# Kernel optimization log

Hardware: AMD Instinct MI355X
Metric: run time of the kernel (lower is better)

## Reference

```python
import jax, jax.numpy as jnp
import numpy as np

N_NODES = 100000
N_EDGES = 1600000
NFEAT = 256
NHID = 128


def setup_inputs() -> dict:
    key = jax.random.key(0)
    ks = jax.random.split(key, 8)
    x = jax.random.normal(ks[0], (N_NODES, NFEAT), dtype=jnp.float32)
    edge_row = jax.random.randint(ks[1], (N_EDGES,), 0, N_NODES, dtype=jnp.int32)
    edge_col = jax.random.randint(ks[2], (N_EDGES,), 0, N_NODES, dtype=jnp.int32)
    edge_val = jax.random.uniform(ks[3], (N_EDGES,), dtype=jnp.float32)
    # Glorot-ish init for the two GraphConvolution weights
    W1 = jax.random.normal(ks[4], (NFEAT, NHID), dtype=jnp.float32) * (1.0 / np.sqrt(NFEAT))
    b1 = jnp.zeros((NHID,), dtype=jnp.float32)
    W2 = jax.random.normal(ks[5], (NHID, NHID), dtype=jnp.float32) * (1.0 / np.sqrt(NHID))
    b2 = jnp.zeros((NHID,), dtype=jnp.float32)
    return {"x": x, "edge_row": edge_row, "edge_col": edge_col,
            "edge_val": edge_val, "W1": W1, "b1": b1, "W2": W2, "b2": b2}


def _gcn_layer(h, W, b, edge_row, edge_col, edge_val, n_nodes):
    # support = h @ W  (dense transform), then spmm(adj, support) + b
    support = h @ W                              # [N, d_out]
    msgs = edge_val[:, None] * support[edge_col]  # [E, d_out] gather
    agg = jax.ops.segment_sum(msgs, edge_row, num_segments=n_nodes)  # scatter-add
    return agg + b


def reference(x, edge_row, edge_col, edge_val, W1, b1, W2, b2):
    n = x.shape[0]
    # eval mode: dropout is identity
    h = jax.nn.relu(_gcn_layer(x, W1, b1, edge_row, edge_col, edge_val, n))
    for _ in range(4):  # gc2 applied 4 times with shared weights
        h = jax.nn.relu(_gcn_layer(h, W2, b2, edge_row, edge_col, edge_val, n))
    return h
```

## Files before the change

kernel.cpp:

```cpp
#include <hip/hip_runtime.h>

constexpr int NFEAT = 256;
constexpr int NHID  = 128;
constexpr int SCAN_B = 4096;


__global__ void hist_kernel(const int* __restrict__ rows, int* __restrict__ cnt, int n) {
  int i = blockIdx.x * blockDim.x + threadIdx.x;
  if (i < n) atomicAdd(&cnt[rows[i]], 1);
}

__global__ void scan1_kernel(const int* __restrict__ cnt, int* __restrict__ part,
                             int* __restrict__ bsum, int n) {
  __shared__ int tmp[1024];
  int tid = threadIdx.x;
  int base = blockIdx.x * SCAN_B + tid * 4;
  int4 v = make_int4(0, 0, 0, 0);
  if (base + 4 <= n) {
    v = *(const int4*)&cnt[base];
  } else {
    if (base + 0 < n) v.x = cnt[base + 0];
    if (base + 1 < n) v.y = cnt[base + 1];
    if (base + 2 < n) v.z = cnt[base + 2];
    if (base + 3 < n) v.w = cnt[base + 3];
  }
  int s = v.x + v.y + v.z + v.w;
  tmp[tid] = s;
  __syncthreads();
  for (int off = 1; off < 1024; off <<= 1) {
    int t = (tid >= off) ? tmp[tid - off] : 0;
    __syncthreads();
    tmp[tid] += t;
    __syncthreads();
  }
  int excl = tmp[tid] - s;
  if (base + 0 < n) part[base + 0] = excl;
  if (base + 1 < n) part[base + 1] = excl + v.x;
  if (base + 2 < n) part[base + 2] = excl + v.x + v.y;
  if (base + 3 < n) part[base + 3] = excl + v.x + v.y + v.z;
  if (tid == 1023) bsum[blockIdx.x] = tmp[1023];
}

__global__ void scan2_kernel(int* __restrict__ bsum, int nb) {
  if (threadIdx.x == 0 && blockIdx.x == 0) {
    int run = 0;
    for (int i = 0; i < nb; ++i) { int t = bsum[i]; bsum[i] = run; run += t; }
    bsum[nb] = run;
  }
}

__global__ void scan3_kernel(int* __restrict__ row_ptr, const int* __restrict__ bsum,
                             int* __restrict__ cursor, int n, int nb) {
  int i = blockIdx.x * blockDim.x + threadIdx.x;
  if (i < n) {
    int v = row_ptr[i] + bsum[i / SCAN_B];
    row_ptr[i] = v;
    cursor[i]  = v;
  }
  if (i == 0) row_ptr[n] = bsum[nb];
}

__global__ void scatter_kernel(const int* __restrict__ rows, const int* __restrict__ cols,
                               const float* __restrict__ vals, int* __restrict__ cursor,
                               int2* __restrict__ ev_s, int n) {
  int i = blockIdx.x * blockDim.x + threadIdx.x;
  if (i < n) {
    int p = atomicAdd(&cursor[rows[i]], 1);
    ev_s[p] = make_int2(cols[i], __float_as_int(vals[i]));
  }
}


__device__ __forceinline__ void gload16(const float* src, float* dst_lds) {
  __builtin_amdgcn_global_load_lds(
      (const __attribute__((address_space(1))) void*)src,
      (__attribute__((address_space(3))) void*)dst_lds,
      16, 0, 0);
}

template<int K>
__global__ __launch_bounds__(256) void gemm_kernel(const float* __restrict__ A,
                                                   const float* __restrict__ W,
                                                   float* __restrict__ C, int M) {
  __shared__ __align__(16) float As[2][2048];
  __shared__ __align__(16) float Bs[2][2048];
  const int tid  = threadIdx.x;
  const int w    = tid >> 6;
  const int lane = tid & 63;
  const int r8   = tid >> 4;
  const int c8   = tid & 15;
  const int block_row = blockIdx.x * 128;

  float acc[2][2][4][4] = {};

  auto prefetch = [&](int t) {
    const int buf = t & 1;
    const int k0  = t * 16;
    #pragma unroll
    for (int j = 0; j < 2; ++j) {
      int s   = j * 256 + w * 64 + lane;
      int row = s >> 2;
      int q   = (s & 3) ^ ((row >> 2) & 3);
      int grow = block_row + row;
      if (grow >= M) grow = M - 1;
      gload16(A + (size_t)grow * K + k0 + q * 4,
              &As[buf][(j * 256 + w * 64) * 4]);
    }
    #pragma unroll
    for (int j = 0; j < 2; ++j) {
      int s = j * 256 + w * 64 + lane;
      int r = s >> 5, cq = s & 31;
      gload16(W + (size_t)(k0 + r) * 128 + cq * 4,
              &Bs[buf][(j * 256 + w * 64) * 4]);
    }
  };

  constexpr int NT = K / 16;
  prefetch(0);
  for (int t = 0; t < NT; ++t) {
    __syncthreads();
    if (t + 1 < NT) prefetch(t + 1);
    const float* as = As[t & 1];
    const float* bs = Bs[t & 1];
    #pragma unroll
    for (int q = 0; q < 4; ++q) {
      float av[2][4][4];
      #pragma unroll
      for (int rh = 0; rh < 2; ++rh)
        #pragma unroll
        for (int i = 0; i < 4; ++i) {
          int row = rh * 64 + r8 * 4 + i;
          float4 a = *(const float4*)&as[(row * 4 + (q ^ ((row >> 2) & 3))) * 4];
          av[rh][i][0] = a.x; av[rh][i][1] = a.y;
          av[rh][i][2] = a.z; av[rh][i][3] = a.w;
        }
      #pragma unroll
      for (int j = 0; j < 4; ++j) {
        int kk = q * 4 + j;
        float4 b0 = *(const float4*)&bs[(kk * 32 + c8) * 4];
        float4 b1 = *(const float4*)&bs[(kk * 32 + 16 + c8) * 4];
        #pragma unroll
        for (int rh = 0; rh < 2; ++rh)
          #pragma unroll
          for (int i = 0; i < 4; ++i) {
            float a = av[rh][i][j];
            acc[rh][0][i][0] += a * b0.x; acc[rh][0][i][1] += a * b0.y;
            acc[rh][0][i][2] += a * b0.z; acc[rh][0][i][3] += a * b0.w;
            acc[rh][1][i][0] += a * b1.x; acc[rh][1][i][1] += a * b1.y;
            acc[rh][1][i][2] += a * b1.z; acc[rh][1][i][3] += a * b1.w;
          }
      }
    }
  }

  #pragma unroll
  for (int rh = 0; rh < 2; ++rh)
    #pragma unroll
    for (int i = 0; i < 4; ++i) {
      int grow = block_row + rh * 64 + r8 * 4 + i;
      if (grow < M) {
        #pragma unroll
        for (int ch = 0; ch < 2; ++ch) {
          float4 v = make_float4(acc[rh][ch][i][0], acc[rh][ch][i][1],
                                 acc[rh][ch][i][2], acc[rh][ch][i][3]);
          *(float4*)&C[(size_t)grow * 128 + ch * 64 + c8 * 4] = v;
        }
      }
    }
}


__global__ void spmm_kernel(const float* __restrict__ support, const int* __restrict__ row_ptr,
                            const int2* __restrict__ ev, const float* __restrict__ bias,
                            float* __restrict__ out, int n_nodes) {
  int row  = blockIdx.x * (blockDim.x >> 6) + (threadIdx.x >> 6);
  int lane = threadIdx.x & 63;
  if (row >= n_nodes) return;
  int beg = row_ptr[row], end = row_ptr[row + 1];
  float ax0 = 0.f, ay0 = 0.f, ax1 = 0.f, ay1 = 0.f;
  for (int chunk = beg; chunk < end; chunk += 64) {
    int idx = chunk + lane;
    int m = min(64, end - chunk);
    int2 ee = (idx < end) ? ev[idx] : make_int2(0, 0);
    int cl = ee.x;
    float vl = __int_as_float(ee.y);
    int e = 0;
    for (; e + 8 <= m; e += 8) {
      int   c0 = __shfl(cl, e + 0), c1 = __shfl(cl, e + 1);
      int   c2 = __shfl(cl, e + 2), c3 = __shfl(cl, e + 3);
      int   c4 = __shfl(cl, e + 4), c5 = __shfl(cl, e + 5);
      int   c6 = __shfl(cl, e + 6), c7 = __shfl(cl, e + 7);
      float v0 = __shfl(vl, e + 0), v1 = __shfl(vl, e + 1);
      float v2 = __shfl(vl, e + 2), v3 = __shfl(vl, e + 3);
      float v4 = __shfl(vl, e + 4), v5 = __shfl(vl, e + 5);
      float v6 = __shfl(vl, e + 6), v7 = __shfl(vl, e + 7);
      float2 s0 = *(const float2*)&support[(size_t)c0 * 128 + lane * 2];
      float2 s1 = *(const float2*)&support[(size_t)c1 * 128 + lane * 2];
      float2 s2 = *(const float2*)&support[(size_t)c2 * 128 + lane * 2];
      float2 s3 = *(const float2*)&support[(size_t)c3 * 128 + lane * 2];
      float2 s4 = *(const float2*)&support[(size_t)c4 * 128 + lane * 2];
      float2 s5 = *(const float2*)&support[(size_t)c5 * 128 + lane * 2];
      float2 s6 = *(const float2*)&support[(size_t)c6 * 128 + lane * 2];
      float2 s7 = *(const float2*)&support[(size_t)c7 * 128 + lane * 2];
      ax0 += v0 * s0.x; ay0 += v0 * s0.y;
      ax1 += v1 * s1.x; ay1 += v1 * s1.y;
      ax0 += v2 * s2.x; ay0 += v2 * s2.y;
      ax1 += v3 * s3.x; ay1 += v3 * s3.y;
      ax0 += v4 * s4.x; ay0 += v4 * s4.y;
      ax1 += v5 * s5.x; ay1 += v5 * s5.y;
      ax0 += v6 * s6.x; ay0 += v6 * s6.y;
      ax1 += v7 * s7.x; ay1 += v7 * s7.y;
    }
    for (; e < m; ++e) {
      int   ce = __shfl(cl, e);
      float ve = __shfl(vl, e);
      float2 s = *(const float2*)&support[(size_t)ce * 128 + lane * 2];
      ax0 += ve * s.x; ay0 += ve * s.y;
    }
  }
  float accx = ax0 + ax1, accy = ay0 + ay1;
  float2 b = *(const float2*)&bias[lane * 2];
  float2 o = make_float2(fmaxf(accx + b.x, 0.f), fmaxf(accy + b.y, 0.f));
  *(float2*)&out[(size_t)row * 128 + lane * 2] = o;
}


extern "C" void kernel_launch(void* const* d_in, const int* in_sizes, int n_in,
                              void* d_out, int out_size, void* d_ws, size_t ws_size,
                              hipStream_t stream) {
  const float* x    = (const float*)d_in[0];
  const int*   erow = (const int*)d_in[1];
  const int*   ecol = (const int*)d_in[2];
  const float* evl  = (const float*)d_in[3];
  const float* W1   = (const float*)d_in[4];
  const float* b1   = (const float*)d_in[5];
  const float* W2   = (const float*)d_in[6];
  const float* b2   = (const float*)d_in[7];
  int n_nodes = in_sizes[0] / NFEAT;
  int n_edges = in_sizes[1];
  float* out = (float*)d_out;

  char* ws = (char*)d_ws;
  size_t off = 0;
  auto alloc = [&](size_t bytes) -> void* {
    void* p = ws + off;
    off += bytes;
    off = (off + 255) & ~(size_t)255;
    return p;
  };
  float* support = (float*)alloc((size_t)n_nodes * NHID * sizeof(float));
  int*   cnt     = (int*)alloc((size_t)n_nodes * sizeof(int));
  int*   row_ptr = (int*)alloc(((size_t)n_nodes + 1) * sizeof(int));
  int*   cursor  = (int*)alloc((size_t)n_nodes * sizeof(int));
  int2*  ev_s    = (int2*)alloc((size_t)n_edges * sizeof(int2));
  int nb = (n_nodes + SCAN_B - 1) / SCAN_B;
  int*   bsum    = (int*)alloc((size_t)(nb + 1) * sizeof(int));

  hipMemsetAsync(cnt, 0, (size_t)n_nodes * sizeof(int), stream);
  hist_kernel<<<(n_edges + 255) / 256, 256, 0, stream>>>(erow, cnt, n_edges);
  scan1_kernel<<<nb, 1024, 0, stream>>>(cnt, row_ptr, bsum, n_nodes);
  scan2_kernel<<<1, 64, 0, stream>>>(bsum, nb);
  scan3_kernel<<<(n_nodes + 255) / 256, 256, 0, stream>>>(row_ptr, bsum, cursor, n_nodes, nb);
  scatter_kernel<<<(n_edges + 255) / 256, 256, 0, stream>>>(erow, ecol, evl, cursor,
                                                            ev_s, n_edges);

  int gblocks = (n_nodes + 127) / 128;
  int sblocks = (n_nodes + 3) / 4;

  gemm_kernel<NFEAT><<<gblocks, 256, 0, stream>>>(x, W1, support, n_nodes);
  spmm_kernel<<<sblocks, 256, 0, stream>>>(support, row_ptr, ev_s, b1, out, n_nodes);

  for (int l = 0; l < 4; ++l) {
    gemm_kernel<NHID><<<gblocks, 256, 0, stream>>>(out, W2, support, n_nodes);
    spmm_kernel<<<sblocks, 256, 0, stream>>>(support, row_ptr, ev_s, b2, out, n_nodes);
  }
}
```

Baseline: 1.054 ms.

## Process two rows per wavefront in SpMM and drop the scatter atomic pass

The SpMM kernel now splits each 64-lane wavefront into two 32-lane halves, each handling one row with float4 gathers, so two rows share one wavefront. With about 16 edges per row on average, this is meant to use lanes better and issue wider loads. The CSR build records each edge's rank from the histogram atomic and computes scatter positions directly, which removes the second atomic pass and the cursor array. In exchange, both halves loop to the larger of their two degrees, which costs some divergence, and an extra per-edge rank array is written and read.

```diff
diff --git a/kernel.cpp b/kernel.cpp
--- a/kernel.cpp
+++ b/kernel.cpp
@@ -5,9 +5,10 @@
 constexpr int SCAN_B = 4096;
 
 
-__global__ void hist_kernel(const int* __restrict__ rows, int* __restrict__ cnt, int n) {
+__global__ void hist_kernel(const int* __restrict__ rows, int* __restrict__ cnt,
+                            int* __restrict__ rank, int n) {
   int i = blockIdx.x * blockDim.x + threadIdx.x;
-  if (i < n) atomicAdd(&cnt[rows[i]], 1);
+  if (i < n) rank[i] = atomicAdd(&cnt[rows[i]], 1);
 }
 
 __global__ void scan1_kernel(const int* __restrict__ cnt, int* __restrict__ part,
@@ -50,22 +51,18 @@
 }
 
 __global__ void scan3_kernel(int* __restrict__ row_ptr, const int* __restrict__ bsum,
-                             int* __restrict__ cursor, int n, int nb) {
+                             int n, int nb) {
+  int i = blockIdx.x * blockDim.x + threadIdx.x;
+  if (i < n) row_ptr[i] += bsum[i / SCAN_B];
+  if (i == 0) row_ptr[n] = bsum[nb];
+}
+
+__global__ void scatter_kernel(const int* __restrict__ rows, const int* __restrict__ cols,
+                               const float* __restrict__ vals, const int* __restrict__ rank,
+                               const int* __restrict__ row_ptr, int2* __restrict__ ev_s, int n) {
   int i = blockIdx.x * blockDim.x + threadIdx.x;
   if (i < n) {
-    int v = row_ptr[i] + bsum[i / SCAN_B];
-    row_ptr[i] = v;
-    cursor[i]  = v;
-  }
-  if (i == 0) row_ptr[n] = bsum[nb];
-}
-
-__global__ void scatter_kernel(const int* __restrict__ rows, const int* __restrict__ cols,
-                               const float* __restrict__ vals, int* __restrict__ cursor,
-                               int2* __restrict__ ev_s, int n) {
-  int i = blockIdx.x * blockDim.x + threadIdx.x;
-  if (i < n) {
-    int p = atomicAdd(&cursor[rows[i]], 1);
+    int p = row_ptr[rows[i]] + rank[i];
     ev_s[p] = make_int2(cols[i], __float_as_int(vals[i]));
   }
 }
@@ -173,55 +170,66 @@
 __global__ void spmm_kernel(const float* __restrict__ support, const int* __restrict__ row_ptr,
                             const int2* __restrict__ ev, const float* __restrict__ bias,
                             float* __restrict__ out, int n_nodes) {
-  int row  = blockIdx.x * (blockDim.x >> 6) + (threadIdx.x >> 6);
-  int lane = threadIdx.x & 63;
-  if (row >= n_nodes) return;
-  int beg = row_ptr[row], end = row_ptr[row + 1];
-  float ax0 = 0.f, ay0 = 0.f, ax1 = 0.f, ay1 = 0.f;
-  for (int chunk = beg; chunk < end; chunk += 64) {
-    int idx = chunk + lane;
-    int m = min(64, end - chunk);
+  int wid   = blockIdx.x * (blockDim.x >> 6) + (threadIdx.x >> 6);
+  int lane  = threadIdx.x & 63;
+  int half  = lane >> 5;
+  int flane = lane & 31;
+  int row   = wid * 2 + half;
+  bool rv   = row < n_nodes;
+  int beg = rv ? row_ptr[row]     : 0;
+  int end = rv ? row_ptr[row + 1] : 0;
+  int deg = end - beg;
+  int mdeg = max(__shfl(deg, 0), __shfl(deg, 32));
+
+  float4 acc = make_float4(0.f, 0.f, 0.f, 0.f);
+  const int sb = half * 32;
+
+  for (int chunk = 0; chunk < mdeg; chunk += 32) {
+    int idx = beg + chunk + flane;
     int2 ee = (idx < end) ? ev[idx] : make_int2(0, 0);
-    int cl = ee.x;
+    int   cl = ee.x;
     float vl = __int_as_float(ee.y);
+    int m = min(32, mdeg - chunk);
     int e = 0;
     for (; e + 8 <= m; e += 8) {
-      int   c0 = __shfl(cl, e + 0), c1 = __shfl(cl, e + 1);
-      int   c2 = __shfl(cl, e + 2), c3 = __shfl(cl, e + 3);
-      int   c4 = __shfl(cl, e + 4), c5 = __shfl(cl, e + 5);
-      int   c6 = __shfl(cl, e + 6), c7 = __shfl(cl, e + 7);
-      float v0 = __shfl(vl, e + 0), v1 = __shfl(vl, e + 1);
-      float v2 = __shfl(vl, e + 2), v3 = __shfl(vl, e + 3);
-      float v4 = __shfl(vl, e + 4), v5 = __shfl(vl, e + 5);
-      float v6 = __shfl(vl, e + 6), v7 = __shfl(vl, e + 7);
-      float2 s0 = *(const float2*)&support[(size_t)c0 * 128 + lane * 2];
-      float2 s1 = *(const float2*)&support[(size_t)c1 * 128 + lane * 2];
-      float2 s2 = *(const float2*)&support[(size_t)c2 * 128 + lane * 2];
-      float2 s3 = *(const float2*)&support[(size_t)c3 * 128 + lane * 2];
-      float2 s4 = *(const float2*)&support[(size_t)c4 * 128 + lane * 2];
-      float2 s5 = *(const float2*)&support[(size_t)c5 * 128 + lane * 2];
-      float2 s6 = *(const float2*)&support[(size_t)c6 * 128 + lane * 2];
-      float2 s7 = *(const float2*)&support[(size_t)c7 * 128 + lane * 2];
-      ax0 += v0 * s0.x; ay0 += v0 * s0.y;
-      ax1 += v1 * s1.x; ay1 += v1 * s1.y;
-      ax0 += v2 * s2.x; ay0 += v2 * s2.y;
-      ax1 += v3 * s3.x; ay1 += v3 * s3.y;
-      ax0 += v4 * s4.x; ay0 += v4 * s4.y;
-      ax1 += v5 * s5.x; ay1 += v5 * s5.y;
-      ax0 += v6 * s6.x; ay0 += v6 * s6.y;
-      ax1 += v7 * s7.x; ay1 += v7 * s7.y;
+      int   c0 = __shfl(cl, sb + e + 0), c1 = __shfl(cl, sb + e + 1);
+      int   c2 = __shfl(cl, sb + e + 2), c3 = __shfl(cl, sb + e + 3);
+      int   c4 = __shfl(cl, sb + e + 4), c5 = __shfl(cl, sb + e + 5);
+      int   c6 = __shfl(cl, sb + e + 6), c7 = __shfl(cl, sb + e + 7);
+      float v0 = __shfl(vl, sb + e + 0), v1 = __shfl(vl, sb + e + 1);
+      float v2 = __shfl(vl, sb + e + 2), v3 = __shfl(vl, sb + e + 3);
+      float v4 = __shfl(vl, sb + e + 4), v5 = __shfl(vl, sb + e + 5);
+      float v6 = __shfl(vl, sb + e + 6), v7 = __shfl(vl, sb + e + 7);
+      float4 s0 = *(const float4*)&support[(size_t)c0 * 128 + flane * 4];
+      float4 s1 = *(const float4*)&support[(size_t)c1 * 128 + flane * 4];
+      float4 s2 = *(const float4*)&support[(size_t)c2 * 128 + flane * 4];
+      float4 s3 = *(const float4*)&support[(size_t)c3 * 128 + flane * 4];
+      float4 s4 = *(const float4*)&support[(size_t)c4 * 128 + flane * 4];
+      float4 s5 = *(const float4*)&support[(size_t)c5 * 128 + flane * 4];
+      float4 s6 = *(const float4*)&support[(size_t)c6 * 128 + flane * 4];
+      float4 s7 = *(const float4*)&support[(size_t)c7 * 128 + flane * 4];
+      acc.x += v0 * s0.x; acc.y += v0 * s0.y; acc.z += v0 * s0.z; acc.w += v0 * s0.w;
+      acc.x += v1 * s1.x; acc.y += v1 * s1.y; acc.z += v1 * s1.z; acc.w += v1 * s1.w;
+      acc.x += v2 * s2.x; acc.y += v2 * s2.y; acc.z += v2 * s2.z; acc.w += v2 * s2.w;
+      acc.x += v3 * s3.x; acc.y += v3 * s3.y; acc.z += v3 * s3.z; acc.w += v3 * s3.w;
+      acc.x += v4 * s4.x; acc.y += v4 * s4.y; acc.z += v4 * s4.z; acc.w += v4 * s4.w;
+      acc.x += v5 * s5.x; acc.y += v5 * s5.y; acc.z += v5 * s5.z; acc.w += v5 * s5.w;
+      acc.x += v6 * s6.x; acc.y += v6 * s6.y; acc.z += v6 * s6.z; acc.w += v6 * s6.w;
+      acc.x += v7 * s7.x; acc.y += v7 * s7.y; acc.z += v7 * s7.z; acc.w += v7 * s7.w;
     }
     for (; e < m; ++e) {
-      int   ce = __shfl(cl, e);
-      float ve = __shfl(vl, e);
-      float2 s = *(const float2*)&support[(size_t)ce * 128 + lane * 2];
-      ax0 += ve * s.x; ay0 += ve * s.y;
-    }
-  }
-  float accx = ax0 + ax1, accy = ay0 + ay1;
-  float2 b = *(const float2*)&bias[lane * 2];
-  float2 o = make_float2(fmaxf(accx + b.x, 0.f), fmaxf(accy + b.y, 0.f));
-  *(float2*)&out[(size_t)row * 128 + lane * 2] = o;
+      int   ce = __shfl(cl, sb + e);
+      float ve = __shfl(vl, sb + e);
+      float4 s = *(const float4*)&support[(size_t)ce * 128 + flane * 4];
+      acc.x += ve * s.x; acc.y += ve * s.y; acc.z += ve * s.z; acc.w += ve * s.w;
+    }
+  }
+  if (rv) {
+    float4 b = *(const float4*)&bias[flane * 4];
+    float4 o = make_float4(fmaxf(acc.x + b.x, 0.f), fmaxf(acc.y + b.y, 0.f),
+                           fmaxf(acc.z + b.z, 0.f), fmaxf(acc.w + b.w, 0.f));
+    *(float4*)&out[(size_t)row * 128 + flane * 4] = o;
+  }
 }
 
 
@@ -251,21 +259,21 @@
   float* support = (float*)alloc((size_t)n_nodes * NHID * sizeof(float));
   int*   cnt     = (int*)alloc((size_t)n_nodes * sizeof(int));
   int*   row_ptr = (int*)alloc(((size_t)n_nodes + 1) * sizeof(int));
-  int*   cursor  = (int*)alloc((size_t)n_nodes * sizeof(int));
+  int*   rank    = (int*)alloc((size_t)n_edges * sizeof(int));
   int2*  ev_s    = (int2*)alloc((size_t)n_edges * sizeof(int2));
   int nb = (n_nodes + SCAN_B - 1) / SCAN_B;
   int*   bsum    = (int*)alloc((size_t)(nb + 1) * sizeof(int));
 
   hipMemsetAsync(cnt, 0, (size_t)n_nodes * sizeof(int), stream);
-  hist_kernel<<<(n_edges + 255) / 256, 256, 0, stream>>>(erow, cnt, n_edges);
+  hist_kernel<<<(n_edges + 255) / 256, 256, 0, stream>>>(erow, cnt, rank, n_edges);
   scan1_kernel<<<nb, 1024, 0, stream>>>(cnt, row_ptr, bsum, n_nodes);
   scan2_kernel<<<1, 64, 0, stream>>>(bsum, nb);
-  scan3_kernel<<<(n_nodes + 255) / 256, 256, 0, stream>>>(row_ptr, bsum, cursor, n_nodes, nb);
-  scatter_kernel<<<(n_edges + 255) / 256, 256, 0, stream>>>(erow, ecol, evl, cursor,
-                                                            ev_s, n_edges);
+  scan3_kernel<<<(n_nodes + 255) / 256, 256, 0, stream>>>(row_ptr, bsum, n_nodes, nb);
+  scatter_kernel<<<(n_edges + 255) / 256, 256, 0, stream>>>(erow, ecol, evl, rank,
+                                                            row_ptr, ev_s, n_edges);
 
   int gblocks = (n_nodes + 127) / 128;
-  int sblocks = (n_nodes + 3) / 4;
+  int sblocks = (n_nodes + 7) / 8;
 
   gemm_kernel<NFEAT><<<gblocks, 256, 0, stream>>>(x, W1, support, n_nodes);
   spmm_kernel<<<sblocks, 256, 0, stream>>>(support, row_ptr, ev_s, b1, out, n_nodes);
```

After: 980.0 us. -7.0%, faster.
